# Performance work log

Hardware: AMD Instinct MI355X
Metric: run time of the kernel (lower is better)

## Reference

```python
import jax, jax.numpy as jnp
import numpy as np

N_NODES = 100000
N_EDGES = 6400000
N_GRAPHS = 512
IN_DIM, HID, OUT = 4, 64, 128


def setup_inputs() -> dict:
    key = jax.random.key(0)
    ks = jax.random.split(key, 6)
    x = jax.random.normal(ks[0], (N_NODES, IN_DIM), dtype=jnp.float32)
    edge_index = jax.random.randint(ks[1], (2, N_EDGES), 0, N_NODES, dtype=jnp.int64)
    batch_ids = jnp.sort(jax.random.randint(ks[2], (N_NODES,), 0, N_GRAPHS, dtype=jnp.int64))
    W1 = jax.random.normal(ks[3], (IN_DIM, HID), dtype=jnp.float32) * (1.0 / np.sqrt(IN_DIM))
    b1 = jnp.zeros((HID,), dtype=jnp.float32)
    W2 = jax.random.normal(ks[4], (HID, HID), dtype=jnp.float32) * (1.0 / np.sqrt(HID))
    b2 = jnp.zeros((HID,), dtype=jnp.float32)
    Wlin = jax.random.normal(ks[5], (HID, OUT), dtype=jnp.float32) * (1.0 / np.sqrt(HID))
    blin = jnp.zeros((OUT,), dtype=jnp.float32)
    return {"x": x, "edge_index": edge_index, "batch_ids": batch_ids,
            "W1": W1, "b1": b1, "W2": W2, "b2": b2, "Wlin": Wlin, "blin": blin}


def reference(x, edge_index, batch_ids, W1, b1, W2, b2, Wlin, blin):
    # GINConv (eps=0): agg[v] = sum_{(u->v) in E} x[u];  h = MLP(x + agg)
    src, dst = edge_index[0], edge_index[1]
    agg = jax.ops.segment_sum(x[src], dst, num_segments=N_NODES)  # [N, in_dim]
    h = x + agg
    h = jax.nn.relu(h @ W1 + b1)  # [N, hid]
    h = h @ W2 + b2               # [N, hid]
    # global mean pool over graphs
    sums = jax.ops.segment_sum(h, batch_ids, num_segments=N_GRAPHS)  # [G, hid]
    counts = jax.ops.segment_sum(jnp.ones((h.shape[0],), dtype=h.dtype), batch_ids,
                                 num_segments=N_GRAPHS)
    pooled = sums / jnp.maximum(counts, 1.0)[:, None]  # [G, hid]
    return pooled @ Wlin + blin  # [G, out]
```

## Files before the change

### kernel.cpp

```cpp
#include <hip/hip_runtime.h>
#include <hip/hip_bf16.h>

#define N_NODES  100000
#define N_EDGES  6400000
#define N_GRAPHS 512
#define HID      64
#define OUT_DIM  128

#define BIN_SHIFT 6
#define BIN_NODES 64
#define NB 1563
#define CAP 5120
#define MAXSEG 8

#define SCB 512
#define SCT 1024
#define SCH (N_EDGES / SCB)
#define SEGB ((NB + 15) / 16)
#define ITERS 13

#define BMT 512
#define NW  8
#define C4 3

__global__ void __launch_bounds__(SCT)
scatter_bin(const int* __restrict__ src, const int* __restrict__ dst,
            unsigned int* __restrict__ cursor, unsigned int* __restrict__ binned) {
    __shared__ unsigned int hist[NB];
    __shared__ unsigned int gbase[NB];
    __shared__ unsigned int sorted[SCH];
    __shared__ unsigned int wtot[16];

    const int tid = threadIdx.x, lane = tid & 63, w = tid >> 6;
    const int e0 = blockIdx.x * SCH;

    int dreg[ITERS], sreg[ITERS];
    #pragma unroll
    for (int k = 0; k < ITERS; ++k) {
        int idx = k * SCT + tid;
        if (idx < SCH) { dreg[k] = dst[e0 + idx]; sreg[k] = src[e0 + idx]; }
        else           { dreg[k] = -1;            sreg[k] = 0; }
    }

    for (int i = tid; i < NB; i += SCT) hist[i] = 0u;
    __syncthreads();

    #pragma unroll
    for (int k = 0; k < ITERS; ++k)
        if (dreg[k] >= 0) atomicAdd(&hist[dreg[k] >> BIN_SHIFT], 1u);
    __syncthreads();

    const int s0 = w * SEGB;
    const int s1 = min(s0 + SEGB, NB);
    unsigned int carry = 0u;
    for (int base = s0; base < s1; base += 64) {
        int i = base + lane;
        bool ok = (i < s1);
        unsigned int v = ok ? hist[i] : 0u;
        if (ok && v)
            gbase[i] = (unsigned int)i * CAP + atomicAdd(&cursor[i], v);
        unsigned int xi = v;
        #pragma unroll
        for (int d = 1; d < 64; d <<= 1) {
            unsigned int u = __shfl_up(xi, d, 64);
            if (lane >= d) xi += u;
        }
        if (ok) hist[i] = carry + xi - v;
        carry += __shfl(xi, 63, 64);
    }
    if (lane == 0) wtot[w] = carry;
    __syncthreads();
    if (w == 0 && lane < 16) {
        unsigned int v = wtot[lane], xi = v;
        #pragma unroll
        for (int d = 1; d < 16; d <<= 1) {
            unsigned int u = __shfl_up(xi, d, 64);
            if (lane >= d) xi += u;
        }
        wtot[lane] = xi - v;
    }
    __syncthreads();
    {
        unsigned int woff = wtot[w];
        for (int i = s0 + lane; i < s1; i += 64) hist[i] += woff;
    }
    __syncthreads();

    #pragma unroll
    for (int k = 0; k < ITERS; ++k) {
        if (dreg[k] >= 0) {
            int b = dreg[k] >> BIN_SHIFT;
            unsigned int slot = atomicAdd(&hist[b], 1u);
            sorted[slot] = ((unsigned int)sreg[k] << BIN_SHIFT)
                         | (unsigned int)(dreg[k] & (BIN_NODES - 1));
        }
    }
    __syncthreads();

    const int sub = lane >> 3, le = lane & 7;
    for (int bb = s0 + sub; bb < s1; bb += 8) {
        unsigned int lo = (bb == 0) ? 0u : hist[bb - 1];
        unsigned int hi = hist[bb];
        unsigned int len = hi - lo;
        if (len == 0u) continue;
        unsigned int gb  = gbase[bb];
        unsigned int end = (unsigned int)(bb + 1) * CAP;
        for (unsigned int t = le; t < len; t += 8)
            if (gb + t < end) binned[gb + t] = sorted[lo + t];
    }
}

__global__ void __launch_bounds__(BMT)
bin_mlp_pool(const unsigned int* __restrict__ binned,
             const unsigned int* __restrict__ cursor,
             const float* __restrict__ x, const int* __restrict__ batch,
             const float* __restrict__ W1, const float* __restrict__ b1,
             float* __restrict__ gsum, float* __restrict__ gcnt) {
    const int b   = blockIdx.x;
    const int n0  = b << BIN_SHIFT;
    const int tid = threadIdx.x;
    const int lane = tid & 63;
    const int w    = tid >> 6;

    __shared__ unsigned int hist[BIN_NODES];
    __shared__ unsigned int off[BIN_NODES + 1];
    __shared__ unsigned int ssrc[CAP];
    __shared__ float lagg[BIN_NODES][4];
    __shared__ float psum[NW][MAXSEG][HID];
    __shared__ float pcnt[NW][MAXSEG];

    if (tid < BIN_NODES) hist[tid] = 0u;
    for (int i = tid; i < NW * MAXSEG * HID; i += BMT) ((float*)psum)[i] = 0.0f;
    if (tid < NW * MAXSEG) ((float*)pcnt)[tid] = 0.0f;
    __syncthreads();

    unsigned int cnt = cursor[b];
    if (cnt > CAP) cnt = CAP;
    const unsigned int* bp = binned + (size_t)b * CAP;

    unsigned int breg[C4][4];
    #pragma unroll
    for (int k = 0; k < C4; ++k) {
        unsigned int i0 = (unsigned int)k * (BMT * 4) + (unsigned int)(tid << 2);
        if (i0 < cnt) {
            uint4 v4 = *reinterpret_cast<const uint4*>(bp + i0);
            breg[k][0] = v4.x; breg[k][1] = v4.y;
            breg[k][2] = v4.z; breg[k][3] = v4.w;
            #pragma unroll
            for (int j = 0; j < 4; ++j) {
                if (i0 + j < cnt) {
                    unsigned int r = atomicAdd(&hist[breg[k][j] & (BIN_NODES - 1)], 1u);
                    breg[k][j] |= (r << 23);
                } else breg[k][j] = 0xFFFFFFFFu;
            }
        } else {
            breg[k][0] = breg[k][1] = breg[k][2] = breg[k][3] = 0xFFFFFFFFu;
        }
    }
    __syncthreads();

    if (tid < BIN_NODES) {
        unsigned int v = hist[tid];
        #pragma unroll
        for (int d = 1; d < 64; d <<= 1) {
            unsigned int u = __shfl_up(v, d, 64);
            if (lane >= d) v += u;
        }
        off[tid + 1] = v;
        if (tid == 0) off[0] = 0u;
    }
    __syncthreads();

    #pragma unroll
    for (int k = 0; k < C4; ++k)
        #pragma unroll
        for (int j = 0; j < 4; ++j) {
            unsigned int e = breg[k][j];
            if (e != 0xFFFFFFFFu) {
                unsigned int dl   = e & (BIN_NODES - 1);
                unsigned int rank = (e >> 23);
                ssrc[off[dl] + rank] = (e >> BIN_SHIFT) & 0x1FFFFu;
            }
        }
    __syncthreads();

    {
        const int sub = lane >> 4, sl = lane & 15;
        #pragma unroll
        for (int r = 0; r < 2; ++r) {
            int dl = w * 8 + r * 4 + sub;
            unsigned int o0 = off[dl], o1 = off[dl + 1];
            float a0 = 0.f, a1 = 0.f, a2 = 0.f, a3 = 0.f;
            for (unsigned int i = o0 + sl; i < o1; i += 16) {
                unsigned int s = ssrc[i];
                float4 xv = *reinterpret_cast<const float4*>(x + (size_t)s * 4);
                a0 += xv.x; a1 += xv.y; a2 += xv.z; a3 += xv.w;
            }
            #pragma unroll
            for (int d = 8; d >= 1; d >>= 1) {
                a0 += __shfl_xor(a0, d, 16);
                a1 += __shfl_xor(a1, d, 16);
                a2 += __shfl_xor(a2, d, 16);
                a3 += __shfl_xor(a3, d, 16);
            }
            if (sl == 0) {
                lagg[dl][0] = a0; lagg[dl][1] = a1;
                lagg[dl][2] = a2; lagg[dl][3] = a3;
            }
        }
    }
    __syncthreads();

    const int j = lane;
    const float w1c0 = W1[0 * HID + j], w1c1 = W1[1 * HID + j];
    const float w1c2 = W1[2 * HID + j], w1c3 = W1[3 * HID + j];
    const float b1j = b1[j];
    const int base_g = batch[n0];

    for (int vl = w * 8; vl < w * 8 + 8; ++vl) {
        int v = n0 + vl;
        if (v >= N_NODES) break;
        float xa0 = x[(size_t)v * 4 + 0] + lagg[vl][0];
        float xa1 = x[(size_t)v * 4 + 1] + lagg[vl][1];
        float xa2 = x[(size_t)v * 4 + 2] + lagg[vl][2];
        float xa3 = x[(size_t)v * 4 + 3] + lagg[vl][3];
        float h = b1j;
        h = fmaf(xa0, w1c0, h);
        h = fmaf(xa1, w1c1, h);
        h = fmaf(xa2, w1c2, h);
        h = fmaf(xa3, w1c3, h);
        h = fmaxf(h, 0.0f);
        int g = batch[v];
        int seg = g - base_g;
        if (seg < MAXSEG) {
            psum[w][seg][j] += h;
            if (j == 0) pcnt[w][seg] += 1.0f;
        } else {
            unsafeAtomicAdd(&gsum[(size_t)g * HID + j], h);
            if (j == 0) unsafeAtomicAdd(&gcnt[g], 1.0f);
        }
    }
    __syncthreads();

    {
        int seg = w;
        float v8 = 0.0f;
        #pragma unroll
        for (int r = 0; r < NW; ++r) v8 += psum[r][seg][j];
        if (v8 != 0.0f)
            unsafeAtomicAdd(&gsum[(size_t)(base_g + seg) * HID + j], v8);
    }
    if (tid < MAXSEG) {
        float c = 0.0f;
        #pragma unroll
        for (int r = 0; r < NW; ++r) c += pcnt[r][tid];
        if (c > 0.0f)
            unsafeAtomicAdd(&gcnt[base_g + tid], c);
    }
}

__global__ void finalize(const float* __restrict__ gsum, const float* __restrict__ gcnt,
                         const float* __restrict__ W2, const float* __restrict__ b2,
                         const float* __restrict__ Wlin, const float* __restrict__ blin,
                         float* __restrict__ out) {
    int g = blockIdx.x;
    int j = threadIdx.x;
    __shared__ float pooled[HID];

    float cnt = gcnt[g];
    float inv = 1.0f / fmaxf(cnt, 1.0f);

    if (j < HID) {
        float s = cnt * b2[j];
        #pragma unroll 8
        for (int k = 0; k < HID; ++k)
            s = fmaf(gsum[(size_t)g * HID + k], W2[k * HID + j], s);
        pooled[j] = s * inv;
    }
    __syncthreads();

    float o = blin[j];
    #pragma unroll 8
    for (int k = 0; k < HID; ++k)
        o = fmaf(pooled[k], Wlin[k * OUT_DIM + j], o);
    out[(size_t)g * OUT_DIM + j] = o;
}

__global__ void edge_scatter(const int* __restrict__ src, const int* __restrict__ dst,
                             const float* __restrict__ x, float* __restrict__ agg) {
    int stride = gridDim.x * blockDim.x;
    for (int e = blockIdx.x * blockDim.x + threadIdx.x; e < N_EDGES; e += stride) {
        int s = src[e];
        int d = dst[e];
        float4 xv = *reinterpret_cast<const float4*>(x + (size_t)s * 4);
        float* a = agg + (size_t)d * 4;
        unsafeAtomicAdd(a + 0, xv.x);
        unsafeAtomicAdd(a + 1, xv.y);
        unsafeAtomicAdd(a + 2, xv.z);
        unsafeAtomicAdd(a + 3, xv.w);
    }
}

__global__ void node_mlp_pool(const float* __restrict__ x, const float* __restrict__ agg,
                              const int* __restrict__ batch,
                              const float* __restrict__ W1, const float* __restrict__ b1,
                              float* __restrict__ gsum, float* __restrict__ gcnt) {
    int j = threadIdx.x & 63;
    int local = threadIdx.x >> 6;
    int v = blockIdx.x * 4 + local;
    if (v >= N_NODES) return;
    float4 xv = *reinterpret_cast<const float4*>(x + (size_t)v * 4);
    float4 av = *reinterpret_cast<const float4*>(agg + (size_t)v * 4);
    float h = b1[j];
    h = fmaf(xv.x + av.x, W1[0 * HID + j], h);
    h = fmaf(xv.y + av.y, W1[1 * HID + j], h);
    h = fmaf(xv.z + av.z, W1[2 * HID + j], h);
    h = fmaf(xv.w + av.w, W1[3 * HID + j], h);
    h = fmaxf(h, 0.0f);
    int g = batch[v];
    unsafeAtomicAdd(&gsum[(size_t)g * HID + j], h);
    if (j == 0) unsafeAtomicAdd(&gcnt[g], 1.0f);
}

extern "C" void kernel_launch(void* const* d_in, const int* in_sizes, int n_in,
                              void* d_out, int out_size, void* d_ws, size_t ws_size,
                              hipStream_t stream) {
    const float* x    = (const float*)d_in[0];
    const int*   ei   = (const int*)d_in[1];
    const int*   bat  = (const int*)d_in[2];
    const float* W1   = (const float*)d_in[3];
    const float* b1   = (const float*)d_in[4];
    const float* W2   = (const float*)d_in[5];
    const float* b2   = (const float*)d_in[6];
    const float* Wlin = (const float*)d_in[7];
    const float* blin = (const float*)d_in[8];
    float* out = (float*)d_out;

    const int* src  = ei;
    const int* dstp = ei + N_EDGES;

    char* ws = (char*)d_ws;
    const size_t GSUM_OFF = 0, GCNT_OFF = 131072, CUR_OFF = 133120, BIN_OFF = 139392;
    const size_t NEED = BIN_OFF + (size_t)NB * CAP * 4 + 16384;

    if (ws_size >= NEED) {
        float* gsum = (float*)(ws + GSUM_OFF);
        float* gcnt = (float*)(ws + GCNT_OFF);
        unsigned int* cursor = (unsigned int*)(ws + CUR_OFF);
        unsigned int* binned = (unsigned int*)(ws + BIN_OFF);

        hipMemsetAsync(d_ws, 0, BIN_OFF, stream);

        scatter_bin<<<SCB, SCT, 0, stream>>>(src, dstp, cursor, binned);
        bin_mlp_pool<<<NB, BMT, 0, stream>>>(binned, cursor, x, bat, W1, b1, gsum, gcnt);
        finalize<<<N_GRAPHS, OUT_DIM, 0, stream>>>(gsum, gcnt, W2, b2, Wlin, blin, out);
    } else {
        float* agg  = (float*)(ws);
        float* gsum = (float*)(ws + 1600000);
        float* gcnt = (float*)(ws + 1600000 + 131072);
        hipMemsetAsync(d_ws, 0, 1600000 + 131072 + 2048, stream);
        edge_scatter<<<4096, 256, 0, stream>>>(src, dstp, x, agg);
        node_mlp_pool<<<(N_NODES + 3) / 4, 256, 0, stream>>>(x, agg, bat, W1, b1, gsum, gcnt);
        finalize<<<N_GRAPHS, OUT_DIM, 0, stream>>>(gsum, gcnt, W2, b2, Wlin, blin, out);
    }
}
```

Baseline: 87.01 us.

## Double bin size to 128 nodes and alias pooling buffer onto edge shared memory

Bins now hold 128 destination nodes, halving the bin count and doubling per-block capacity and per-wave node work. The scan becomes a chunked wave scan, the rank field is shifted to 24 bits, and slot indices are bounds-checked. The per-wave pooling partial sums now reuse the edge-source shared array instead of a separate buffer, which keeps LDS usage in check. The intent is fewer blocks with longer edge runs and less scatter fragmentation. The cost is more registers (C4=5), possibly lower occupancy, and an extra barrier.

```diff
diff --git a/kernel.cpp b/kernel.cpp
--- a/kernel.cpp
+++ b/kernel.cpp
@@ -7,10 +7,10 @@
 #define HID      64
 #define OUT_DIM  128
 
-#define BIN_SHIFT 6
-#define BIN_NODES 64
-#define NB 1563
-#define CAP 5120
+#define BIN_SHIFT 7
+#define BIN_NODES 128
+#define NB 782
+#define CAP 9984
 #define MAXSEG 8
 
 #define SCB 512
@@ -21,7 +21,7 @@
 
 #define BMT 512
 #define NW  8
-#define C4 3
+#define C4 5
 
 __global__ void __launch_bounds__(SCT)
 scatter_bin(const int* __restrict__ src, const int* __restrict__ dst,
@@ -97,15 +97,15 @@
     }
     __syncthreads();
 
-    const int sub = lane >> 3, le = lane & 7;
-    for (int bb = s0 + sub; bb < s1; bb += 8) {
+    const int sub = lane >> 4, le = lane & 15;
+    for (int bb = s0 + sub; bb < s1; bb += 4) {
         unsigned int lo = (bb == 0) ? 0u : hist[bb - 1];
         unsigned int hi = hist[bb];
         unsigned int len = hi - lo;
         if (len == 0u) continue;
         unsigned int gb  = gbase[bb];
         unsigned int end = (unsigned int)(bb + 1) * CAP;
-        for (unsigned int t = le; t < len; t += 8)
+        for (unsigned int t = le; t < len; t += 16)
             if (gb + t < end) binned[gb + t] = sorted[lo + t];
     }
 }
@@ -126,11 +126,10 @@
     __shared__ unsigned int off[BIN_NODES + 1];
     __shared__ unsigned int ssrc[CAP];
     __shared__ float lagg[BIN_NODES][4];
-    __shared__ float psum[NW][MAXSEG][HID];
     __shared__ float pcnt[NW][MAXSEG];
+    float* psum = (float*)ssrc;
 
     if (tid < BIN_NODES) hist[tid] = 0u;
-    for (int i = tid; i < NW * MAXSEG * HID; i += BMT) ((float*)psum)[i] = 0.0f;
     if (tid < NW * MAXSEG) ((float*)pcnt)[tid] = 0.0f;
     __syncthreads();
 
@@ -150,7 +149,7 @@
             for (int j = 0; j < 4; ++j) {
                 if (i0 + j < cnt) {
                     unsigned int r = atomicAdd(&hist[breg[k][j] & (BIN_NODES - 1)], 1u);
-                    breg[k][j] |= (r << 23);
+                    breg[k][j] |= (r << 24);
                 } else breg[k][j] = 0xFFFFFFFFu;
             }
         } else {
@@ -159,15 +158,21 @@
     }
     __syncthreads();
 
-    if (tid < BIN_NODES) {
-        unsigned int v = hist[tid];
-        #pragma unroll
-        for (int d = 1; d < 64; d <<= 1) {
-            unsigned int u = __shfl_up(v, d, 64);
-            if (lane >= d) v += u;
-        }
-        off[tid + 1] = v;
-        if (tid == 0) off[0] = 0u;
+    if (w == 0) {
+        unsigned int carry = 0u;
+        #pragma unroll
+        for (int base = 0; base < BIN_NODES; base += 64) {
+            unsigned int v = hist[base + lane];
+            unsigned int xi = v;
+            #pragma unroll
+            for (int d = 1; d < 64; d <<= 1) {
+                unsigned int u = __shfl_up(xi, d, 64);
+                if (lane >= d) xi += u;
+            }
+            off[base + lane + 1] = carry + xi;
+            carry += __shfl(xi, 63, 64);
+        }
+        if (lane == 0) off[0] = 0u;
     }
     __syncthreads();
 
@@ -178,8 +183,9 @@
             unsigned int e = breg[k][j];
             if (e != 0xFFFFFFFFu) {
                 unsigned int dl   = e & (BIN_NODES - 1);
-                unsigned int rank = (e >> 23);
-                ssrc[off[dl] + rank] = (e >> BIN_SHIFT) & 0x1FFFFu;
+                unsigned int rank = e >> 24;
+                unsigned int slot = off[dl] + rank;
+                if (slot < CAP) ssrc[slot] = (e >> BIN_SHIFT) & 0x1FFFFu;
             }
         }
     __syncthreads();
@@ -187,9 +193,10 @@
     {
         const int sub = lane >> 4, sl = lane & 15;
         #pragma unroll
-        for (int r = 0; r < 2; ++r) {
-            int dl = w * 8 + r * 4 + sub;
-            unsigned int o0 = off[dl], o1 = off[dl + 1];
+        for (int r = 0; r < 4; ++r) {
+            int dl = w * 16 + r * 4 + sub;
+            unsigned int o0 = min(off[dl],     (unsigned int)CAP);
+            unsigned int o1 = min(off[dl + 1], (unsigned int)CAP);
             float a0 = 0.f, a1 = 0.f, a2 = 0.f, a3 = 0.f;
             for (unsigned int i = o0 + sl; i < o1; i += 16) {
                 unsigned int s = ssrc[i];
@@ -211,13 +218,16 @@
     }
     __syncthreads();
 
+    for (int i = tid; i < NW * MAXSEG * HID; i += BMT) psum[i] = 0.0f;
+    __syncthreads();
+
     const int j = lane;
     const float w1c0 = W1[0 * HID + j], w1c1 = W1[1 * HID + j];
     const float w1c2 = W1[2 * HID + j], w1c3 = W1[3 * HID + j];
     const float b1j = b1[j];
     const int base_g = batch[n0];
 
-    for (int vl = w * 8; vl < w * 8 + 8; ++vl) {
+    for (int vl = w * 16; vl < w * 16 + 16; ++vl) {
         int v = n0 + vl;
         if (v >= N_NODES) break;
         float xa0 = x[(size_t)v * 4 + 0] + lagg[vl][0];
@@ -233,7 +243,7 @@
         int g = batch[v];
         int seg = g - base_g;
         if (seg < MAXSEG) {
-            psum[w][seg][j] += h;
+            psum[(w * MAXSEG + seg) * HID + j] += h;
             if (j == 0) pcnt[w][seg] += 1.0f;
         } else {
             unsafeAtomicAdd(&gsum[(size_t)g * HID + j], h);
@@ -246,7 +256,7 @@
         int seg = w;
         float v8 = 0.0f;
         #pragma unroll
-        for (int r = 0; r < NW; ++r) v8 += psum[r][seg][j];
+        for (int r = 0; r < NW; ++r) v8 += psum[(r * MAXSEG + seg) * HID + j];
         if (v8 != 0.0f)
             unsafeAtomicAdd(&gsum[(size_t)(base_g + seg) * HID + j], v8);
     }
@@ -340,7 +350,7 @@
     const int* dstp = ei + N_EDGES;
 
     char* ws = (char*)d_ws;
-    const size_t GSUM_OFF = 0, GCNT_OFF = 131072, CUR_OFF = 133120, BIN_OFF = 139392;
+    const size_t GSUM_OFF = 0, GCNT_OFF = 131072, CUR_OFF = 133120, BIN_OFF = 136320;
     const size_t NEED = BIN_OFF + (size_t)NB * CAP * 4 + 16384;
 
     if (ws_size >= NEED) {
```

After: 95.40 us. +9.6%, slower.
